# Performance work log

Hardware: AMD Instinct MI355X
Metric: run time of the kernel (lower is better)

## Reference

```python
import jax, jax.numpy as jnp
import numpy as np

CTX = 2048   # context_window
D   = 256    # emb_dim
B   = 16     # batch
C   = 2048   # sequence length (<= CTX)


def make_rotary_matrix(ctx, d):
    """Dense per-position rotation matrix, as in the tinyllama get_rotary_matrix:
    theta_i = 10000 ** (-2*(i-1)/d), 2x2 rotation blocks on the diagonal."""
    pos = np.arange(ctx, dtype=np.float64)[:, None]            # [ctx, 1]
    i = np.arange(d // 2, dtype=np.float64)                    # [d/2]
    theta = 10000.0 ** (-2.0 * (i - 1.0) / d)                  # note (i-1), matches source
    ang = pos * theta                                          # [ctx, d/2]
    c, s = np.cos(ang), np.sin(ang)
    R = np.zeros((ctx, d, d), dtype=np.float32)
    k = np.arange(d // 2)
    R[:, 2 * k, 2 * k] = c
    R[:, 2 * k, 2 * k + 1] = -s
    R[:, 2 * k + 1, 2 * k] = s
    R[:, 2 * k + 1, 2 * k + 1] = c
    return jnp.asarray(R)


def setup_inputs() -> dict:
    key = jax.random.key(0)
    ks = jax.random.split(key, 4)
    scale = 1.0 / np.sqrt(D)
    x = jax.random.normal(ks[0], (B, C, D), dtype=jnp.float32)
    Wq = jax.random.normal(ks[1], (D, D), dtype=jnp.float32) * scale
    Wk = jax.random.normal(ks[2], (D, D), dtype=jnp.float32) * scale
    Wv = jax.random.normal(ks[3], (D, D), dtype=jnp.float32) * scale
    bq = jnp.zeros((D,), dtype=jnp.float32)
    bk = jnp.zeros((D,), dtype=jnp.float32)
    bv = jnp.zeros((D,), dtype=jnp.float32)
    R = make_rotary_matrix(CTX, D)
    return {"x": x, "Wq": Wq, "bq": bq, "Wk": Wk, "bk": bk, "Wv": Wv, "bv": bv, "R": R}


def reference(x, Wq, bq, Wk, bk, Wv, bv, R):
    Bz, Cz, d = x.shape
    # QKV projections (torch Linear: y = x @ W.T + b)
    q = x @ Wq.T + bq
    k = x @ Wk.T + bk
    v = x @ Wv.T + bv
    # Dense rotary: q_rot[b,c,:] = R[c] @ q[b,c,:]  (original: bmm(q^T, R[:C]^T)^T)
    Rc = R[:Cz]                                        # [C, D, D]
    q_rot = jnp.einsum('bcd,ced->bce', q, Rc)          # [B, C, D]
    k_rot = jnp.einsum('bcd,ced->bce', k, Rc)          # [B, C, D]
    # Causal SDPA (dropout_p=0.2 in source -> disabled here, eval-mode determinism)
    scale = 1.0 / jnp.sqrt(jnp.asarray(d, dtype=x.dtype))
    scores = jnp.einsum('bqd,bkd->bqk', q_rot, k_rot) * scale   # [B, C, C]
    causal = jnp.tril(jnp.ones((Cz, Cz), dtype=bool))
    scores = jnp.where(causal, scores, jnp.asarray(-jnp.inf, dtype=scores.dtype))
    attn = jax.nn.softmax(scores, axis=-1)
    out = jnp.einsum('bqk,bkd->bqd', attn, v)                   # [B, C, D]
    return out
```

## Files before the change

kernel.cpp:

```cpp
#include <hip/hip_runtime.h>
#include <stdint.h>

#define BB 16
#define CC 2048
#define DD 256
#define MM (BB*CC)

typedef __attribute__((ext_vector_type(4))) float f32x4;
typedef __attribute__((ext_vector_type(8))) short bf16x8;
typedef __attribute__((ext_vector_type(4))) short s16x4;

static __device__ __forceinline__ short f2bf(float f) {
  union { float f; uint32_t u; } v; v.f = f;
  uint32_t u = v.u;
  return (short)((u + 0x7FFFu + ((u >> 16) & 1u)) >> 16);
}

#define GLDS16(gp, lp) __builtin_amdgcn_global_load_lds(                      \
    (const __attribute__((address_space(1))) void*)(gp),                      \
    (__attribute__((address_space(3))) void*)(lp), 16, 0, 0)

#define DPP_ROR_F(x, n) __uint_as_float(__builtin_amdgcn_update_dpp(          \
    0, (int)__float_as_uint(x), 0x120 + (n), 0xF, 0xF, false))

__global__ __launch_bounds__(256) void k_prep(
    const float* __restrict__ Wq, const float* __restrict__ Wk,
    const float* __restrict__ Wv, short* __restrict__ wb,
    float2* __restrict__ cs) {
  const int bid = blockIdx.x;
  if (bid < 64) {
    int id = bid * 256 + threadIdx.x;
    int k = id & 127, pg = id >> 7;
    double th = pow(10000.0, (1.0 - (double)k) * (1.0 / 128.0));
    const double TWO_PI = 6.283185307179586476925287;
    const double INV_2PI = 1.0 / TWO_PI;
    #pragma unroll
    for (int i = 0; i < 16; ++i) {
      int pos = pg * 16 + i;
      double ang = (double)pos * th;
      double red = ang - floor(ang * INV_2PI) * TWO_PI;
      float fr = (float)red;
      cs[(size_t)pos * 128 + k] = make_float2(__cosf(fr), __sinf(fr));
    }
  } else {
    int gid = (bid - 64) * 256 + threadIdx.x;
    int s = gid / 3072;
    int og = gid - s * 3072;
    int mat = og >> 10;
    int o = (og & 1023) * 8;
    int e_local = o >> 6;
    int e = (s & 1) * 128 + e_local;
    int kc = s >> 1;
    int c4 = ((o & 63) ^ (((e >> 1) & 3) << 4)) >> 3;
    const float* W = (mat == 0) ? Wq : (mat == 1) ? Wk : Wv;
    f32x4 wv = *(const f32x4*)(W + (size_t)e * DD + kc * 32 + c4 * 4);
    s16x4 b4;
    b4[0] = f2bf(wv[0]); b4[1] = f2bf(wv[1]); b4[2] = f2bf(wv[2]); b4[3] = f2bf(wv[3]);
    *(s16x4*)((char*)wb + (size_t)gid * 8) = b4;
  }
}

__global__ __launch_bounds__(256, 2) void k_qkv(
    const float* __restrict__ x, const short* __restrict__ wb,
    const float* __restrict__ bq, const float* __restrict__ bk,
    const float* __restrict__ bv, const float2* __restrict__ cs,
    short* __restrict__ q_rot, short* __restrict__ k_rot,
    short* __restrict__ v_t)
{
  __shared__ char SM[81920];
  short* xs = (short*)SM;
  char* wsh = SM + 32768;
  const int t = threadIdx.x;
  const int lane = t & 63, w = t >> 6;
  const int g = lane >> 4, li = lane & 15;
  const int m0 = blockIdx.x * 64;

  #pragma unroll
  for (int i = 0; i < 16; ++i) {
    int chunk = i * 256 + t;
    int row = chunk >> 6, c4 = chunk & 63;
    f32x4 xv = *(const f32x4*)(x + (size_t)(m0 + row) * DD + c4 * 4);
    s16x4 b4;
    b4[0] = f2bf(xv[0]); b4[1] = f2bf(xv[1]); b4[2] = f2bf(xv[2]); b4[3] = f2bf(xv[3]);
    *(s16x4*)((char*)xs + row * 512 + ((c4 * 8) ^ ((row & 7) << 4))) = b4;
  }

  auto STAGE = [&](int buf, int s) {
    #pragma unroll
    for (int i = 0; i < 6; ++i) {
      int cc = i * 4 + w;
      const char* src = (const char*)wb + s * 24576 + cc * 1024 + lane * 16;
      GLDS16(src, wsh + buf * 24576 + cc * 1024);
    }
  };

  STAGE(0, 0);
  __syncthreads();

  f32x4 zero4 = {0.f, 0.f, 0.f, 0.f};
  f32x4 accQ[16], accK[16], accV[16];
  #pragma unroll
  for (int nt = 0; nt < 16; ++nt) { accQ[nt] = zero4; accK[nt] = zero4; accV[nt] = zero4; }

  #pragma unroll
  for (int kc = 0; kc < 8; ++kc) {
    #pragma unroll
    for (int eh = 0; eh < 2; ++eh) {
      const int s = kc * 2 + eh;
      asm volatile("s_waitcnt vmcnt(0)" ::: "memory");
      __builtin_amdgcn_sched_barrier(0);
      __builtin_amdgcn_s_barrier();
      if (s + 1 < 16) STAGE((s + 1) & 1, s + 1);

      const int arow = w * 16 + li;
      bf16x8 a = *(const bf16x8*)((char*)xs + arow * 512 +
                                  (((kc * 64) + g * 16) ^ ((arow & 7) << 4)));
      const char* Wb = wsh + (s & 1) * 24576;
      #pragma unroll
      for (int ntl = 0; ntl < 8; ++ntl) {
        const int nt = eh * 8 + ntl;
        int e_local = ntl * 16 + li;
        int off = e_local * 64 + ((g * 16) ^ (((e_local >> 1) & 3) << 4));
        bf16x8 fq = *(const bf16x8*)(Wb + off);
        bf16x8 fk = *(const bf16x8*)(Wb + 8192 + off);
        bf16x8 fv = *(const bf16x8*)(Wb + 16384 + off);
        accQ[nt] = __builtin_amdgcn_mfma_f32_16x16x32_bf16(a, fq, accQ[nt], 0, 0, 0);
        accK[nt] = __builtin_amdgcn_mfma_f32_16x16x32_bf16(a, fk, accK[nt], 0, 0, 0);
        accV[nt] = __builtin_amdgcn_mfma_f32_16x16x32_bf16(a, fv, accV[nt], 0, 0, 0);
      }
    }
  }

  __syncthreads();
  {
    char* Tq = SM;
    char* Tk = SM + 33792;
    #pragma unroll
    for (int nt = 0; nt < 16; ++nt) {
      int e = nt * 16 + li;
      float bQ = bq[e], bK = bk[e];
      #pragma unroll
      for (int r = 0; r < 4; ++r) {
        int cloc = w * 16 + g * 4 + r;
        int m = m0 + cloc;
        float2 csv = cs[(size_t)(m & (CC - 1)) * 128 + (e >> 1)];
        float vq = accQ[nt][r] + bQ;
        float oq = __shfl_xor(vq, 1);
        vq = csv.x * vq + ((e & 1) ? csv.y * oq : -csv.y * oq);
        *(short*)(Tq + cloc * 528 + e * 2) = f2bf(vq * 0.0625f);
        float vk = accK[nt][r] + bK;
        float ok = __shfl_xor(vk, 1);
        vk = csv.x * vk + ((e & 1) ? csv.y * ok : -csv.y * ok);
        *(short*)(Tk + cloc * 528 + e * 2) = f2bf(vk);
      }
    }
    __syncthreads();
    #pragma unroll
    for (int it = 0; it < 8; ++it) {
      int chunk = it * 256 + t;
      int c = chunk >> 5, e32 = chunk & 31;
      int4 vq4 = *(const int4*)(Tq + c * 528 + e32 * 16);
      int4 vk4 = *(const int4*)(Tk + c * 528 + e32 * 16);
      *(int4*)(q_rot + (size_t)(m0 + c) * DD + e32 * 8) = vq4;
      *(int4*)(k_rot + (size_t)(m0 + c) * DD + e32 * 8) = vk4;
    }
  }
  __syncthreads();
  #pragma unroll
  for (int nt = 0; nt < 16; ++nt) {
    int e = nt * 16 + li;
    float bias = bv[e];
    #pragma unroll
    for (int r = 0; r < 4; ++r) {
      int cloc = w * 16 + g * 4 + r;
      *(short*)(SM + e * 144 + cloc * 2) = f2bf(accV[nt][r] + bias);
    }
  }
  __syncthreads();
  {
    const int bb = m0 >> 11, c0 = m0 & (CC - 1);
    #pragma unroll
    for (int it = 0; it < 8; ++it) {
      int chunk = it * 256 + t;
      int e = chunk >> 3, c8 = chunk & 7;
      int4 vv = *(const int4*)(SM + e * 144 + c8 * 16);
      *(int4*)(v_t + ((size_t)(bb * DD + e)) * CC + c0 + c8 * 8) = vv;
    }
  }
}

__global__ __launch_bounds__(512, 2) void k_attn(
    const short* __restrict__ q_rot, const short* __restrict__ k_rot,
    const short* __restrict__ v_t, float* __restrict__ out)
{
  __shared__ char SM[143360];
  const int t = threadIdx.x;
  const int lane = t & 63, w = t >> 6;
  const int wg = w & 3, gq = w >> 2;
  const int g = lane >> 4, li = lane & 15;

  const int p = blockIdx.x;
  const int b = p & 15;
  const int j = p >> 4;

  const short* kbase = k_rot + (size_t)b * CC * DD;
  const short* vbase = v_t  + (size_t)b * DD * CC;

  float* U  = (float*)(SM + 65536);
  float* ML = (float*)(SM + 142848);
  char* Pb = SM + 132608 + w * 1280;

  f32x4 zero4 = {0.f, 0.f, 0.f, 0.f};

  for (int tt = 0; tt < 2; ++tt) {
    const int qt = tt ? (31 - j) : j;
    const int q0 = qt * 64;
    const int NTg = qt + 1;
    const int kvoff = gq * 32 * NTg;

    const short* qb = q_rot + ((size_t)b * CC + q0 + wg * 16 + li) * DD;
    bf16x8 qf[8];
    #pragma unroll
    for (int dc = 0; dc < 8; ++dc)
      qf[dc] = *(const bf16x8*)(qb + dc * 32 + g * 8);

    f32x4 O[16];
    #pragma unroll
    for (int i = 0; i < 16; ++i) O[i] = zero4;
    float mrow[4], lrow[4];
    #pragma unroll
    for (int r = 0; r < 4; ++r) { mrow[r] = -__builtin_inff(); lrow[r] = 0.f; }

    auto STAGE = [&](int buf, int kt) {
      const int k0s = kvoff + kt * 32;
      char* dst = SM + (size_t)(gq * 2 + buf) * 32768;
      #pragma unroll
      for (int i = 0; i < 4; ++i) {
        int c = i * 4 + wg;
        int row = 2 * c + (lane >> 5);
        int cb = ((lane & 31) * 16) ^ ((row & 7) << 4);
        const char* src = (const char*)(kbase + (size_t)(k0s + row) * DD) + cb;
        GLDS16(src, dst + c * 1024);
      }
      #pragma unroll
      for (int i = 0; i < 4; ++i) {
        int c = i * 4 + wg;
        int d = 16 * c + (lane >> 2);
        int sb = (((lane & 3) ^ ((lane >> 3) & 3)) * 16);
        const char* src = (const char*)(vbase + (size_t)d * CC + k0s) + sb;
        GLDS16(src, dst + 16384 + c * 1024);
      }
    };

    int cur = 0;
    STAGE(0, 0);
    for (int kt = 0; kt < NTg; ++kt) {
      const int k0 = kvoff + kt * 32;
      asm volatile("s_waitcnt vmcnt(0)" ::: "memory");
      __builtin_amdgcn_sched_barrier(0);
      __builtin_amdgcn_s_barrier();
      if (kt + 1 < NTg) STAGE(cur ^ 1, kt + 1);

      const char* Kb = SM + (size_t)(gq * 2 + cur) * 32768;
      const char* Vb = Kb + 16384;

      f32x4 S[2];
      S[0] = zero4; S[1] = zero4;
      __builtin_amdgcn_s_setprio(1);
      #pragma unroll
      for (int dc = 0; dc < 8; ++dc) {
        #pragma unroll
        for (int nt = 0; nt < 2; ++nt) {
          int krow = nt * 16 + li;
          bf16x8 kf = *(const bf16x8*)(Kb + krow * 512 +
                                       (((dc * 64) + g * 16) ^ ((krow & 7) << 4)));
          S[nt] = __builtin_amdgcn_mfma_f32_16x16x32_bf16(qf[dc], kf, S[nt], 0, 0, 0);
        }
      }
      __builtin_amdgcn_s_setprio(0);

      if (k0 + 31 > q0) {
        #pragma unroll
        for (int nt = 0; nt < 2; ++nt)
          #pragma unroll
          for (int r = 0; r < 4; ++r)
            if ((k0 + nt * 16 + li) > (q0 + wg * 16 + g * 4 + r))
              S[nt][r] = -1.0e30f;
      }

      float mxr[4];
      #pragma unroll
      for (int r = 0; r < 4; ++r) {
        float mx = fmaxf(S[0][r], S[1][r]);
        mx = fmaxf(mx, DPP_ROR_F(mx, 8));
        mx = fmaxf(mx, DPP_ROR_F(mx, 4));
        mx = fmaxf(mx, DPP_ROR_F(mx, 2));
        mx = fmaxf(mx, DPP_ROR_F(mx, 1));
        mxr[r] = mx;
      }
      int need = 0;
      #pragma unroll
      for (int r = 0; r < 4; ++r) need |= (mxr[r] > mrow[r] + 8.f) ? 1 : 0;
      if (__any(need)) {
        #pragma unroll
        for (int r = 0; r < 4; ++r) {
          float mnew = fmaxf(mrow[r], mxr[r]);
          float al = __expf(mrow[r] - mnew);
          mrow[r] = mnew;
          lrow[r] *= al;
          #pragma unroll
          for (int dt2 = 0; dt2 < 16; ++dt2) O[dt2][r] *= al;
        }
      }
      #pragma unroll
      for (int r = 0; r < 4; ++r) {
        float rsum = 0.f;
        #pragma unroll
        for (int nt = 0; nt < 2; ++nt) {
          float pv = __expf(S[nt][r] - mrow[r]);
          S[nt][r] = pv;
          rsum += pv;
        }
        rsum += DPP_ROR_F(rsum, 8);
        rsum += DPP_ROR_F(rsum, 4);
        rsum += DPP_ROR_F(rsum, 2);
        rsum += DPP_ROR_F(rsum, 1);
        lrow[r] += rsum;
      }

      #pragma unroll
      for (int nt = 0; nt < 2; ++nt)
        #pragma unroll
        for (int r = 0; r < 4; ++r)
          *(short*)(Pb + (g * 4 + r) * 80 + (nt * 16 + li) * 2) = f2bf(S[nt][r]);

      bf16x8 pf = *(const bf16x8*)(Pb + li * 80 + g * 16);

      __builtin_amdgcn_s_setprio(1);
      #pragma unroll
      for (int dt2 = 0; dt2 < 16; ++dt2) {
        bf16x8 vf = *(const bf16x8*)(Vb + (dt2 * 16 + li) * 64 +
                                     ((g * 16) ^ (((li >> 1) & 3) << 4)));
        O[dt2] = __builtin_amdgcn_mfma_f32_16x16x32_bf16(pf, vf, O[dt2], 0, 0, 0);
      }
      __builtin_amdgcn_s_setprio(0);
      cur ^= 1;
    }

    __syncthreads();
    if (gq == 1) {
      #pragma unroll
      for (int r = 0; r < 4; ++r) {
        int row = wg * 16 + g * 4 + r;
        if (li == 0) { ML[row * 2] = mrow[r]; ML[row * 2 + 1] = lrow[r]; }
        #pragma unroll
        for (int dt2 = 0; dt2 < 16; ++dt2)
          U[row * 260 + dt2 * 16 + li] = O[dt2][r];
      }
    }
    __syncthreads();
    if (gq == 0) {
      float eA[4], eB[4], invl[4];
      #pragma unroll
      for (int r = 0; r < 4; ++r) {
        int row = wg * 16 + g * 4 + r;
        float mB = ML[row * 2], lB = ML[row * 2 + 1];
        float m = fmaxf(mrow[r], mB);
        eA[r] = __expf(mrow[r] - m);
        eB[r] = __expf(mB - m);
        invl[r] = 1.f / (lrow[r] * eA[r] + lB * eB[r]);
      }
      #pragma unroll
      for (int dt2 = 0; dt2 < 16; ++dt2)
        #pragma unroll
        for (int r = 0; r < 4; ++r) {
          int row = wg * 16 + g * 4 + r;
          float uB = U[row * 260 + dt2 * 16 + li];
          out[((size_t)b * CC + q0 + row) * DD + dt2 * 16 + li] =
              (O[dt2][r] * eA[r] + uB * eB[r]) * invl[r];
        }
    }
    __syncthreads();
  }
}

extern "C" void kernel_launch(void* const* d_in, const int* in_sizes, int n_in,
                              void* d_out, int out_size, void* d_ws, size_t ws_size,
                              hipStream_t stream) {
  const float* x  = (const float*)d_in[0];
  const float* Wq = (const float*)d_in[1];
  const float* bq = (const float*)d_in[2];
  const float* Wk = (const float*)d_in[3];
  const float* bk = (const float*)d_in[4];
  const float* Wv = (const float*)d_in[5];
  const float* bv = (const float*)d_in[6];
  float* out = (float*)d_out;
  (void)in_sizes; (void)n_in; (void)out_size; (void)ws_size;

  char* ws = (char*)d_ws;
  float2* cs   = (float2*)ws;
  short* q_rot = (short*)(ws + (2u << 20));
  short* k_rot = q_rot + (size_t)MM * DD;
  short* v_tr  = k_rot + (size_t)MM * DD;
  short* wb    = v_tr + (size_t)MM * DD;

  k_prep <<< 256, 256, 0, stream>>>(Wq, Wk, Wv, wb, cs);
  k_qkv  <<< 512, 256, 0, stream>>>(x, wb, bq, bk, bv, cs, q_rot, k_rot, v_tr);
  k_attn <<< 256, 512, 0, stream>>>(q_rot, k_rot, v_tr, out);
}
```

Baseline: 118.0 us.

## Warp-specialize attention into QK-softmax and PV wave groups pipelined by one tile

Splits the eight waves of each block into two roles. Four waves compute QK^T and the online softmax for 32 query rows each, writing P tiles and rescale factors into double-buffered LDS. The other four waves consume them one tile later to accumulate P·V. K and V staging are separated so that V for tile t and K for tile t+1 load while compute proceeds. This aims to overlap softmax and exp work with the PV MFMAs, at the cost of more LDS, more barrier traffic, and doubled accumulator registers per PV wave.

```diff
diff --git a/kernel.cpp b/kernel.cpp
--- a/kernel.cpp
+++ b/kernel.cpp
@@ -193,11 +193,14 @@
     const short* __restrict__ q_rot, const short* __restrict__ k_rot,
     const short* __restrict__ v_t, float* __restrict__ out)
 {
-  __shared__ char SM[143360];
-  const int t = threadIdx.x;
-  const int lane = t & 63, w = t >> 6;
-  const int wg = w & 3, gq = w >> 2;
+  __shared__ char SM[153664];
+  const int t_ = threadIdx.x;
+  const int lane = t_ & 63, w = t_ >> 6;
   const int g = lane >> 4, li = lane & 15;
+  const bool isQK = (w < 4);
+  const int sub = (w >> 1) & 1;
+  const int grp = w & 1;
+  const int ws = w >> 1;
 
   const int p = blockIdx.x;
   const int b = p & 15;
@@ -206,9 +209,8 @@
   const short* kbase = k_rot + (size_t)b * CC * DD;
   const short* vbase = v_t  + (size_t)b * DD * CC;
 
-  float* U  = (float*)(SM + 65536);
-  float* ML = (float*)(SM + 142848);
-  char* Pb = SM + 132608 + w * 1280;
+  float* U  = (float*)SM;
+  float* ML = (float*)(SM + 152640);
 
   f32x4 zero4 = {0.f, 0.f, 0.f, 0.f};
 
@@ -216,171 +218,247 @@
     const int qt = tt ? (31 - j) : j;
     const int q0 = qt * 64;
     const int NTg = qt + 1;
-    const int kvoff = gq * 32 * NTg;
-
-    const short* qb = q_rot + ((size_t)b * CC + q0 + wg * 16 + li) * DD;
-    bf16x8 qf[8];
-    #pragma unroll
-    for (int dc = 0; dc < 8; ++dc)
-      qf[dc] = *(const bf16x8*)(qb + dc * 32 + g * 8);
-
-    f32x4 O[16];
-    #pragma unroll
-    for (int i = 0; i < 16; ++i) O[i] = zero4;
-    float mrow[4], lrow[4];
-    #pragma unroll
-    for (int r = 0; r < 4; ++r) { mrow[r] = -__builtin_inff(); lrow[r] = 0.f; }
-
-    auto STAGE = [&](int buf, int kt) {
+    const int kvoff = grp * 32 * NTg;
+
+    char* Kg = SM + grp * 32768;
+    char* Vg = SM + 65536 + grp * 32768;
+    char* Pg = SM + 131072 + grp * 10240;
+    char* Ag = SM + 151552 + grp * 544;
+
+    auto STAGE_K = [&](int buf, int kt) {
       const int k0s = kvoff + kt * 32;
-      char* dst = SM + (size_t)(gq * 2 + buf) * 32768;
+      char* dst = Kg + buf * 16384;
       #pragma unroll
       for (int i = 0; i < 4; ++i) {
-        int c = i * 4 + wg;
+        int c = i * 4 + ws;
         int row = 2 * c + (lane >> 5);
         int cb = ((lane & 31) * 16) ^ ((row & 7) << 4);
         const char* src = (const char*)(kbase + (size_t)(k0s + row) * DD) + cb;
         GLDS16(src, dst + c * 1024);
       }
+    };
+    auto STAGE_V = [&](int buf, int kt) {
+      const int k0s = kvoff + kt * 32;
+      char* dst = Vg + buf * 16384;
       #pragma unroll
       for (int i = 0; i < 4; ++i) {
-        int c = i * 4 + wg;
+        int c = i * 4 + ws;
         int d = 16 * c + (lane >> 2);
         int sb = (((lane & 3) ^ ((lane >> 3) & 3)) * 16);
         const char* src = (const char*)(vbase + (size_t)d * CC + k0s) + sb;
-        GLDS16(src, dst + 16384 + c * 1024);
+        GLDS16(src, dst + 16384 * 0 + c * 1024);
       }
     };
 
-    int cur = 0;
-    STAGE(0, 0);
-    for (int kt = 0; kt < NTg; ++kt) {
-      const int k0 = kvoff + kt * 32;
-      asm volatile("s_waitcnt vmcnt(0)" ::: "memory");
-      __builtin_amdgcn_sched_barrier(0);
-      __builtin_amdgcn_s_barrier();
-      if (kt + 1 < NTg) STAGE(cur ^ 1, kt + 1);
-
-      const char* Kb = SM + (size_t)(gq * 2 + cur) * 32768;
-      const char* Vb = Kb + 16384;
-
-      f32x4 S[2];
-      S[0] = zero4; S[1] = zero4;
-      __builtin_amdgcn_s_setprio(1);
-      #pragma unroll
-      for (int dc = 0; dc < 8; ++dc) {
-        #pragma unroll
-        for (int nt = 0; nt < 2; ++nt) {
-          int krow = nt * 16 + li;
-          bf16x8 kf = *(const bf16x8*)(Kb + krow * 512 +
-                                       (((dc * 64) + g * 16) ^ ((krow & 7) << 4)));
-          S[nt] = __builtin_amdgcn_mfma_f32_16x16x32_bf16(qf[dc], kf, S[nt], 0, 0, 0);
+    if (isQK) {
+      bf16x8 qf[2][8];
+      #pragma unroll
+      for (int rb = 0; rb < 2; ++rb) {
+        const short* qb = q_rot + ((size_t)b * CC + q0 + sub * 32 + rb * 16 + li) * DD;
+        #pragma unroll
+        for (int dc = 0; dc < 8; ++dc)
+          qf[rb][dc] = *(const bf16x8*)(qb + dc * 32 + g * 8);
+      }
+      float mrow[2][4], lrow[2][4];
+      #pragma unroll
+      for (int rb = 0; rb < 2; ++rb)
+        #pragma unroll
+        for (int r = 0; r < 4; ++r) { mrow[rb][r] = -__builtin_inff(); lrow[rb][r] = 0.f; }
+
+      STAGE_K(0, 0);
+      for (int t = 0; t <= NTg; ++t) {
+        asm volatile("s_waitcnt vmcnt(0) lgkmcnt(0)" ::: "memory");
+        __builtin_amdgcn_sched_barrier(0);
+        __builtin_amdgcn_s_barrier();
+        if (t < NTg) STAGE_V(t & 1, t);
+        if (t + 1 < NTg) STAGE_K((t + 1) & 1, t + 1);
+
+        if (t < NTg) {
+          const int k0 = kvoff + t * 32;
+          const char* Kb = Kg + (t & 1) * 16384;
+          f32x4 S[2][2];
+          S[0][0] = zero4; S[0][1] = zero4; S[1][0] = zero4; S[1][1] = zero4;
+          __builtin_amdgcn_s_setprio(1);
+          #pragma unroll
+          for (int dc = 0; dc < 8; ++dc) {
+            #pragma unroll
+            for (int nt = 0; nt < 2; ++nt) {
+              int krow = nt * 16 + li;
+              bf16x8 kf = *(const bf16x8*)(Kb + krow * 512 +
+                                           (((dc * 64) + g * 16) ^ ((krow & 7) << 4)));
+              S[0][nt] = __builtin_amdgcn_mfma_f32_16x16x32_bf16(qf[0][dc], kf, S[0][nt], 0, 0, 0);
+              S[1][nt] = __builtin_amdgcn_mfma_f32_16x16x32_bf16(qf[1][dc], kf, S[1][nt], 0, 0, 0);
+            }
+          }
+          __builtin_amdgcn_s_setprio(0);
+
+          if (k0 + 31 > q0 + sub * 32) {
+            #pragma unroll
+            for (int rb = 0; rb < 2; ++rb)
+              #pragma unroll
+              for (int nt = 0; nt < 2; ++nt)
+                #pragma unroll
+                for (int r = 0; r < 4; ++r)
+                  if ((k0 + nt * 16 + li) > (q0 + sub * 32 + rb * 16 + g * 4 + r))
+                    S[rb][nt][r] = -1.0e30f;
+          }
+
+          char* Pb = Pg + (t & 1) * 5120;
+          char* Ab = Ag + (t & 1) * 272;
+          int fb = 0;
+          #pragma unroll
+          for (int rb = 0; rb < 2; ++rb) {
+            float mxr[4];
+            #pragma unroll
+            for (int r = 0; r < 4; ++r) {
+              float mx = fmaxf(S[rb][0][r], S[rb][1][r]);
+              mx = fmaxf(mx, DPP_ROR_F(mx, 8));
+              mx = fmaxf(mx, DPP_ROR_F(mx, 4));
+              mx = fmaxf(mx, DPP_ROR_F(mx, 2));
+              mx = fmaxf(mx, DPP_ROR_F(mx, 1));
+              mxr[r] = mx;
+            }
+            int need = 0;
+            #pragma unroll
+            for (int r = 0; r < 4; ++r) need |= (mxr[r] > mrow[rb][r] + 8.f) ? 1 : 0;
+            if (__any(need)) {
+              fb |= (1 << rb);
+              #pragma unroll
+              for (int r = 0; r < 4; ++r) {
+                float mnew = fmaxf(mrow[rb][r], mxr[r]);
+                float al = __expf(mrow[rb][r] - mnew);
+                mrow[rb][r] = mnew;
+                lrow[rb][r] *= al;
+                if (li == 0)
+                  *(float*)(Ab + (sub * 32 + rb * 16 + g * 4 + r) * 4) = al;
+              }
+            }
+            #pragma unroll
+            for (int r = 0; r < 4; ++r) {
+              float pv0 = __expf(S[rb][0][r] - mrow[rb][r]);
+              float pv1 = __expf(S[rb][1][r] - mrow[rb][r]);
+              S[rb][0][r] = pv0; S[rb][1][r] = pv1;
+              float rsum = pv0 + pv1;
+              rsum += DPP_ROR_F(rsum, 8);
+              rsum += DPP_ROR_F(rsum, 4);
+              rsum += DPP_ROR_F(rsum, 2);
+              rsum += DPP_ROR_F(rsum, 1);
+              lrow[rb][r] += rsum;
+            }
+            #pragma unroll
+            for (int nt = 0; nt < 2; ++nt)
+              #pragma unroll
+              for (int r = 0; r < 4; ++r)
+                *(short*)(Pb + (sub * 32 + rb * 16 + g * 4 + r) * 80 +
+                          (nt * 16 + li) * 2) = f2bf(S[rb][nt][r]);
+          }
+          if (lane == 0) *(int*)(Ab + 256 + sub * 4) = fb;
         }
       }
-      __builtin_amdgcn_s_setprio(0);
-
-      if (k0 + 31 > q0) {
-        #pragma unroll
-        for (int nt = 0; nt < 2; ++nt)
-          #pragma unroll
-          for (int r = 0; r < 4; ++r)
-            if ((k0 + nt * 16 + li) > (q0 + wg * 16 + g * 4 + r))
-              S[nt][r] = -1.0e30f;
-      }
-
-      float mxr[4];
-      #pragma unroll
-      for (int r = 0; r < 4; ++r) {
-        float mx = fmaxf(S[0][r], S[1][r]);
-        mx = fmaxf(mx, DPP_ROR_F(mx, 8));
-        mx = fmaxf(mx, DPP_ROR_F(mx, 4));
-        mx = fmaxf(mx, DPP_ROR_F(mx, 2));
-        mx = fmaxf(mx, DPP_ROR_F(mx, 1));
-        mxr[r] = mx;
-      }
-      int need = 0;
-      #pragma unroll
-      for (int r = 0; r < 4; ++r) need |= (mxr[r] > mrow[r] + 8.f) ? 1 : 0;
-      if (__any(need)) {
-        #pragma unroll
-        for (int r = 0; r < 4; ++r) {
-          float mnew = fmaxf(mrow[r], mxr[r]);
-          float al = __expf(mrow[r] - mnew);
-          mrow[r] = mnew;
-          lrow[r] *= al;
-          #pragma unroll
-          for (int dt2 = 0; dt2 < 16; ++dt2) O[dt2][r] *= al;
+      __syncthreads();
+      if (li == 0) {
+        #pragma unroll
+        for (int rb = 0; rb < 2; ++rb)
+          #pragma unroll
+          for (int r = 0; r < 4; ++r) {
+            int row = sub * 32 + rb * 16 + g * 4 + r;
+            ML[grp * 128 + row * 2]     = mrow[rb][r];
+            ML[grp * 128 + row * 2 + 1] = lrow[rb][r];
+          }
+      }
+      __syncthreads();
+      __syncthreads();
+    } else {
+      f32x4 O[2][16];
+      #pragma unroll
+      for (int rb = 0; rb < 2; ++rb)
+        #pragma unroll
+        for (int i = 0; i < 16; ++i) O[rb][i] = zero4;
+
+      STAGE_K(0, 0);
+      for (int t = 0; t <= NTg; ++t) {
+        asm volatile("s_waitcnt vmcnt(0) lgkmcnt(0)" ::: "memory");
+        __builtin_amdgcn_sched_barrier(0);
+        __builtin_amdgcn_s_barrier();
+        if (t < NTg) STAGE_V(t & 1, t);
+        if (t + 1 < NTg) STAGE_K((t + 1) & 1, t + 1);
+
+        if (t >= 1) {
+          const int bb2 = (t - 1) & 1;
+          const char* Vb = Vg + bb2 * 16384;
+          const char* Pb = Pg + bb2 * 5120;
+          const char* Ab = Ag + bb2 * 272;
+          int fb = *(const int*)(Ab + 256 + sub * 4);
+          if (fb & 1) {
+            #pragma unroll
+            for (int r = 0; r < 4; ++r) {
+              float a = *(const float*)(Ab + (sub * 32 + g * 4 + r) * 4);
+              #pragma unroll
+              for (int dt2 = 0; dt2 < 16; ++dt2) O[0][dt2][r] *= a;
+            }
+          }
+          if (fb & 2) {
+            #pragma unroll
+            for (int r = 0; r < 4; ++r) {
+              float a = *(const float*)(Ab + (sub * 32 + 16 + g * 4 + r) * 4);
+              #pragma unroll
+              for (int dt2 = 0; dt2 < 16; ++dt2) O[1][dt2][r] *= a;
+            }
+          }
+          bf16x8 pf0 = *(const bf16x8*)(Pb + (sub * 32 + li) * 80 + g * 16);
+          bf16x8 pf1 = *(const bf16x8*)(Pb + (sub * 32 + 16 + li) * 80 + g * 16);
+          __builtin_amdgcn_s_setprio(1);
+          #pragma unroll
+          for (int dt2 = 0; dt2 < 16; ++dt2) {
+            int vrow = dt2 * 16 + li;
+            bf16x8 vf = *(const bf16x8*)(Vb + vrow * 64 +
+                                         ((g * 16) ^ (((li >> 1) & 3) << 4)));
+            O[0][dt2] = __builtin_amdgcn_mfma_f32_16x16x32_bf16(pf0, vf, O[0][dt2], 0, 0, 0);
+            O[1][dt2] = __builtin_amdgcn_mfma_f32_16x16x32_bf16(pf1, vf, O[1][dt2], 0, 0, 0);
+          }
+          __builtin_amdgcn_s_setprio(0);
         }
       }
-      #pragma unroll
-      for (int r = 0; r < 4; ++r) {
-        float rsum = 0.f;
-        #pragma unroll
-        for (int nt = 0; nt < 2; ++nt) {
-          float pv = __expf(S[nt][r] - mrow[r]);
-          S[nt][r] = pv;
-          rsum += pv;
+      __syncthreads();
+      if (grp == 1) {
+        #pragma unroll
+        for (int rb = 0; rb < 2; ++rb)
+          #pragma unroll
+          for (int r = 0; r < 4; ++r) {
+            int row = sub * 32 + rb * 16 + g * 4 + r;
+            #pragma unroll
+            for (int dt2 = 0; dt2 < 16; ++dt2)
+              U[row * 260 + dt2 * 16 + li] = O[rb][dt2][r];
+          }
+      }
+      __syncthreads();
+      if (grp == 0) {
+        #pragma unroll
+        for (int rb = 0; rb < 2; ++rb) {
+          float eA[4], eB[4], invl[4];
+          #pragma unroll
+          for (int r = 0; r < 4; ++r) {
+            int row = sub * 32 + rb * 16 + g * 4 + r;
+            float m0_ = ML[row * 2], l0_ = ML[row * 2 + 1];
+            float m1_ = ML[128 + row * 2], l1_ = ML[128 + row * 2 + 1];
+            float M = fmaxf(m0_, m1_);
+            eA[r] = __expf(m0_ - M);
+            eB[r] = __expf(m1_ - M);
+            invl[r] = 1.f / (l0_ * eA[r] + l1_ * eB[r]);
+          }
+          #pragma unroll
+          for (int dt2 = 0; dt2 < 16; ++dt2)
+            #pragma unroll
+            for (int r = 0; r < 4; ++r) {
+              int row = sub * 32 + rb * 16 + g * 4 + r;
+              float uB = U[row * 260 + dt2 * 16 + li];
+              out[((size_t)b * CC + q0 + row) * DD + dt2 * 16 + li] =
+                  (O[rb][dt2][r] * eA[r] + uB * eB[r]) * invl[r];
+            }
         }
-        rsum += DPP_ROR_F(rsum, 8);
-        rsum += DPP_ROR_F(rsum, 4);
-        rsum += DPP_ROR_F(rsum, 2);
-        rsum += DPP_ROR_F(rsum, 1);
-        lrow[r] += rsum;
-      }
-
-      #pragma unroll
-      for (int nt = 0; nt < 2; ++nt)
-        #pragma unroll
-        for (int r = 0; r < 4; ++r)
-          *(short*)(Pb + (g * 4 + r) * 80 + (nt * 16 + li) * 2) = f2bf(S[nt][r]);
-
-      bf16x8 pf = *(const bf16x8*)(Pb + li * 80 + g * 16);
-
-      __builtin_amdgcn_s_setprio(1);
-      #pragma unroll
-      for (int dt2 = 0; dt2 < 16; ++dt2) {
-        bf16x8 vf = *(const bf16x8*)(Vb + (dt2 * 16 + li) * 64 +
-                                     ((g * 16) ^ (((li >> 1) & 3) << 4)));
-        O[dt2] = __builtin_amdgcn_mfma_f32_16x16x32_bf16(pf, vf, O[dt2], 0, 0, 0);
-      }
-      __builtin_amdgcn_s_setprio(0);
-      cur ^= 1;
-    }
-
-    __syncthreads();
-    if (gq == 1) {
-      #pragma unroll
-      for (int r = 0; r < 4; ++r) {
-        int row = wg * 16 + g * 4 + r;
-        if (li == 0) { ML[row * 2] = mrow[r]; ML[row * 2 + 1] = lrow[r]; }
-        #pragma unroll
-        for (int dt2 = 0; dt2 < 16; ++dt2)
-          U[row * 260 + dt2 * 16 + li] = O[dt2][r];
-      }
-    }
-    __syncthreads();
-    if (gq == 0) {
-      float eA[4], eB[4], invl[4];
-      #pragma unroll
-      for (int r = 0; r < 4; ++r) {
-        int row = wg * 16 + g * 4 + r;
-        float mB = ML[row * 2], lB = ML[row * 2 + 1];
-        float m = fmaxf(mrow[r], mB);
-        eA[r] = __expf(mrow[r] - m);
-        eB[r] = __expf(mB - m);
-        invl[r] = 1.f / (lrow[r] * eA[r] + lB * eB[r]);
-      }
-      #pragma unroll
-      for (int dt2 = 0; dt2 < 16; ++dt2)
-        #pragma unroll
-        for (int r = 0; r < 4; ++r) {
-          int row = wg * 16 + g * 4 + r;
-          float uB = U[row * 260 + dt2 * 16 + li];
-          out[((size_t)b * CC + q0 + row) * DD + dt2 * 16 + li] =
-              (O[dt2][r] * eA[r] + uB * eB[r]) * invl[r];
-        }
-    }
-    __syncthreads();
+      }
+      __syncthreads();
+    }
   }
 }
 
```

Measured after the change: 120.6 us. 2.2% more time.

## Retile QKV projection so each wave owns output columns across all rows

Applied to the files above, without the earlier changes.

Each wave now computes all 64 rows for a quarter of the output columns instead of 16 rows for all columns, so every B fragment loaded from LDS feeds four MFMAs rather than one. This cuts LDS reads of the weight tile. The epilogue drops the LDS transpose staging and writes q_rot, k_rot and v_t directly from registers. In exchange the global stores become scattered 2-byte (q/k) and 8-byte (v) writes instead of coalesced 16-byte ones, and the cos/sin loads are less contiguous.

```diff
diff --git a/kernel.cpp b/kernel.cpp
--- a/kernel.cpp
+++ b/kernel.cpp
@@ -98,93 +98,87 @@
   __syncthreads();
 
   f32x4 zero4 = {0.f, 0.f, 0.f, 0.f};
-  f32x4 accQ[16], accK[16], accV[16];
+  f32x4 acc[3][4][4];
   #pragma unroll
-  for (int nt = 0; nt < 16; ++nt) { accQ[nt] = zero4; accK[nt] = zero4; accV[nt] = zero4; }
+  for (int m = 0; m < 3; ++m)
+    #pragma unroll
+    for (int s = 0; s < 4; ++s)
+      #pragma unroll
+      for (int rt = 0; rt < 4; ++rt) acc[m][s][rt] = zero4;
 
   #pragma unroll
   for (int kc = 0; kc < 8; ++kc) {
     #pragma unroll
     for (int eh = 0; eh < 2; ++eh) {
-      const int s = kc * 2 + eh;
+      const int st = kc * 2 + eh;
       asm volatile("s_waitcnt vmcnt(0)" ::: "memory");
       __builtin_amdgcn_sched_barrier(0);
       __builtin_amdgcn_s_barrier();
-      if (s + 1 < 16) STAGE((s + 1) & 1, s + 1);
-
-      const int arow = w * 16 + li;
-      bf16x8 a = *(const bf16x8*)((char*)xs + arow * 512 +
-                                  (((kc * 64) + g * 16) ^ ((arow & 7) << 4)));
-      const char* Wb = wsh + (s & 1) * 24576;
-      #pragma unroll
-      for (int ntl = 0; ntl < 8; ++ntl) {
-        const int nt = eh * 8 + ntl;
-        int e_local = ntl * 16 + li;
-        int off = e_local * 64 + ((g * 16) ^ (((e_local >> 1) & 3) << 4));
-        bf16x8 fq = *(const bf16x8*)(Wb + off);
-        bf16x8 fk = *(const bf16x8*)(Wb + 8192 + off);
-        bf16x8 fv = *(const bf16x8*)(Wb + 16384 + off);
-        accQ[nt] = __builtin_amdgcn_mfma_f32_16x16x32_bf16(a, fq, accQ[nt], 0, 0, 0);
-        accK[nt] = __builtin_amdgcn_mfma_f32_16x16x32_bf16(a, fk, accK[nt], 0, 0, 0);
-        accV[nt] = __builtin_amdgcn_mfma_f32_16x16x32_bf16(a, fv, accV[nt], 0, 0, 0);
-      }
-    }
-  }
-
-  __syncthreads();
-  {
-    char* Tq = SM;
-    char* Tk = SM + 33792;
-    #pragma unroll
-    for (int nt = 0; nt < 16; ++nt) {
-      int e = nt * 16 + li;
-      float bQ = bq[e], bK = bk[e];
-      #pragma unroll
-      for (int r = 0; r < 4; ++r) {
-        int cloc = w * 16 + g * 4 + r;
-        int m = m0 + cloc;
-        float2 csv = cs[(size_t)(m & (CC - 1)) * 128 + (e >> 1)];
-        float vq = accQ[nt][r] + bQ;
-        float oq = __shfl_xor(vq, 1);
-        vq = csv.x * vq + ((e & 1) ? csv.y * oq : -csv.y * oq);
-        *(short*)(Tq + cloc * 528 + e * 2) = f2bf(vq * 0.0625f);
-        float vk = accK[nt][r] + bK;
-        float ok = __shfl_xor(vk, 1);
-        vk = csv.x * vk + ((e & 1) ? csv.y * ok : -csv.y * ok);
-        *(short*)(Tk + cloc * 528 + e * 2) = f2bf(vk);
-      }
-    }
-    __syncthreads();
-    #pragma unroll
-    for (int it = 0; it < 8; ++it) {
-      int chunk = it * 256 + t;
-      int c = chunk >> 5, e32 = chunk & 31;
-      int4 vq4 = *(const int4*)(Tq + c * 528 + e32 * 16);
-      int4 vk4 = *(const int4*)(Tk + c * 528 + e32 * 16);
-      *(int4*)(q_rot + (size_t)(m0 + c) * DD + e32 * 8) = vq4;
-      *(int4*)(k_rot + (size_t)(m0 + c) * DD + e32 * 8) = vk4;
-    }
-  }
-  __syncthreads();
+      if (st + 1 < 16) STAGE((st + 1) & 1, st + 1);
+
+      const char* Wb = wsh + (st & 1) * 24576;
+
+      bf16x8 a[4];
+      #pragma unroll
+      for (int rt = 0; rt < 4; ++rt) {
+        int arow = rt * 16 + li;
+        a[rt] = *(const bf16x8*)((char*)xs + arow * 512 +
+                                 (((kc * 64) + g * 16) ^ ((arow & 7) << 4)));
+      }
+      #pragma unroll
+      for (int m = 0; m < 3; ++m) {
+        #pragma unroll
+        for (int ss = 0; ss < 2; ++ss) {
+          int ctl = w + 4 * ss;
+          int e_local = ctl * 16 + li;
+          int off = m * 8192 + e_local * 64 +
+                    ((g * 16) ^ (((li >> 1) & 3) << 4));
+          bf16x8 bf = *(const bf16x8*)(Wb + off);
+          acc[m][eh * 2 + ss][0] = __builtin_amdgcn_mfma_f32_16x16x32_bf16(a[0], bf, acc[m][eh * 2 + ss][0], 0, 0, 0);
+          acc[m][eh * 2 + ss][1] = __builtin_amdgcn_mfma_f32_16x16x32_bf16(a[1], bf, acc[m][eh * 2 + ss][1], 0, 0, 0);
+          acc[m][eh * 2 + ss][2] = __builtin_amdgcn_mfma_f32_16x16x32_bf16(a[2], bf, acc[m][eh * 2 + ss][2], 0, 0, 0);
+          acc[m][eh * 2 + ss][3] = __builtin_amdgcn_mfma_f32_16x16x32_bf16(a[3], bf, acc[m][eh * 2 + ss][3], 0, 0, 0);
+        }
+      }
+    }
+  }
+
   #pragma unroll
-  for (int nt = 0; nt < 16; ++nt) {
-    int e = nt * 16 + li;
-    float bias = bv[e];
-    #pragma unroll
-    for (int r = 0; r < 4; ++r) {
-      int cloc = w * 16 + g * 4 + r;
-      *(short*)(SM + e * 144 + cloc * 2) = f2bf(accV[nt][r] + bias);
-    }
-  }
-  __syncthreads();
+  for (int m = 0; m < 2; ++m) {
+    short* dst = m ? k_rot : q_rot;
+    const float* bp = m ? bk : bq;
+    const float qs = m ? 1.0f : 0.0625f;
+    #pragma unroll
+    for (int s = 0; s < 4; ++s) {
+      int e = (w + 4 * s) * 16 + li;
+      float bias = bp[e];
+      #pragma unroll
+      for (int rt = 0; rt < 4; ++rt) {
+        #pragma unroll
+        for (int r = 0; r < 4; ++r) {
+          int mr = m0 + rt * 16 + g * 4 + r;
+          float2 csv = cs[(size_t)(mr & (CC - 1)) * 128 + (e >> 1)];
+          float val = acc[m][s][rt][r] + bias;
+          float other = __shfl_xor(val, 1);
+          val = csv.x * val + ((e & 1) ? csv.y * other : -csv.y * other);
+          dst[(size_t)mr * DD + e] = f2bf(val * qs);
+        }
+      }
+    }
+  }
   {
     const int bb = m0 >> 11, c0 = m0 & (CC - 1);
     #pragma unroll
-    for (int it = 0; it < 8; ++it) {
-      int chunk = it * 256 + t;
-      int e = chunk >> 3, c8 = chunk & 7;
-      int4 vv = *(const int4*)(SM + e * 144 + c8 * 16);
-      *(int4*)(v_t + ((size_t)(bb * DD + e)) * CC + c0 + c8 * 8) = vv;
+    for (int s = 0; s < 4; ++s) {
+      int e = (w + 4 * s) * 16 + li;
+      float bias = bv[e];
+      #pragma unroll
+      for (int rt = 0; rt < 4; ++rt) {
+        s16x4 o4;
+        #pragma unroll
+        for (int r = 0; r < 4; ++r) o4[r] = f2bf(acc[2][s][rt][r] + bias);
+        *(s16x4*)(v_t + ((size_t)(bb * DD + e)) * CC + c0 + rt * 16 + g * 4) = o4;
+      }
     }
   }
 }
```

Result: slower. 139.1 us (+17.9%).
